# Kernel optimization log

Hardware: AMD Instinct MI355X
Metric: run time of the kernel (lower is better)

Reference implementation:

```python
import jax, jax.numpy as jnp
import numpy as np

N, E, F_IN, EDIM, HEADS, DIM = 100000, 1600000, 128, 16, 4, 16
HC = HEADS * DIM


def add_self_loops_mean(src, dst, ea, n):
    # PyG add_self_loops with fill_value='mean': self-loop edge_attr is the mean
    # of incoming-edge attrs per target node (0 for isolated nodes).
    cnt = jax.ops.segment_sum(jnp.ones((dst.shape[0],), ea.dtype), dst, num_segments=n)
    sm = jax.ops.segment_sum(ea, dst, num_segments=n)
    loop = jnp.where(cnt[:, None] > 0, sm / jnp.maximum(cnt, 1.0)[:, None], 0.0)
    idx = jnp.arange(n, dtype=src.dtype)
    return (jnp.concatenate([src, idx]), jnp.concatenate([dst, idx]),
            jnp.concatenate([ea, loop], axis=0))


def gatv2(x, src, dst, ea, Wl, bl, Wr, br, We, att, bias):
    n = x.shape[0]
    h, c = att.shape
    xl = (x @ Wl + bl).reshape(n, h, c)   # source transform (lin_l)
    xr = (x @ Wr + br).reshape(n, h, c)   # target transform (lin_r)
    ee = (ea @ We).reshape(-1, h, c)      # edge transform (lin_edge, no bias)
    s = jax.nn.leaky_relu(xl[src] + xr[dst] + ee, negative_slope=0.2)  # [E,h,c]
    alpha = jnp.einsum('ehc,hc->eh', s, att)                           # [E,h]
    amax = jax.ops.segment_max(alpha, dst, num_segments=n)
    amax = jnp.where(jnp.isfinite(amax), amax, 0.0)
    ex = jnp.exp(alpha - amax[dst])
    denom = jax.ops.segment_sum(ex, dst, num_segments=n)
    a = ex / (denom[dst] + 1e-16)                                      # segment softmax
    out = jax.ops.segment_sum(xl[src] * a[:, :, None], dst, num_segments=n)
    return out.reshape(n, h * c) + bias


def setup_inputs() -> dict:
    key = jax.random.key(0)
    ks = jax.random.split(key, 24)
    s = 0.1
    d = {
        'x': jax.random.normal(ks[0], (N, F_IN), jnp.float32),
        'edge_index': jax.random.randint(ks[1], (2, E), 0, N, jnp.int32),
        'edge_attr': jax.random.normal(ks[2], (E, EDIM), jnp.float32),
        'Wl1': jax.random.normal(ks[3], (F_IN, HC)) * s, 'bl1': jnp.zeros((HC,)),
        'Wr1': jax.random.normal(ks[4], (F_IN, HC)) * s, 'br1': jnp.zeros((HC,)),
        'We1': jax.random.normal(ks[5], (EDIM, HC)) * s,
        'att1': jax.random.normal(ks[6], (HEADS, DIM)) * s,
        'bias1': jnp.zeros((HC,)),
        'Wl2': jax.random.normal(ks[7], (HC, HC)) * s, 'bl2': jnp.zeros((HC,)),
        'Wr2': jax.random.normal(ks[8], (HC, HC)) * s, 'br2': jnp.zeros((HC,)),
        'We2': jax.random.normal(ks[9], (EDIM, HC)) * s,
        'att2': jax.random.normal(ks[10], (HEADS, DIM)) * s,
        'bias2': jnp.zeros((HC,)),
        'W_lin1': jax.random.normal(ks[11], (HC, DIM)) * s, 'b_lin1': jnp.zeros((DIM,)),
        'W_lin2': jax.random.normal(ks[12], (DIM, 1)) * s, 'b_lin2': jnp.zeros((1,)),
    }
    return d


def reference(x, edge_index, edge_attr, Wl1, bl1, Wr1, br1, We1, att1, bias1,
              Wl2, bl2, Wr2, br2, We2, att2, bias2,
              W_lin1, b_lin1, W_lin2, b_lin2):
    src, dst, ea = add_self_loops_mean(edge_index[0], edge_index[1], edge_attr, x.shape[0])
    h = jax.nn.relu(gatv2(x, src, dst, ea, Wl1, bl1, Wr1, br1, We1, att1, bias1))
    h = jax.nn.relu(gatv2(h, src, dst, ea, Wl2, bl2, Wr2, br2, We2, att2, bias2))
    h = jax.nn.relu(h @ W_lin1 + b_lin1)
    # dropout p=0.1 is identity in eval mode
    out = jax.nn.sigmoid((h @ W_lin2 + b_lin2)[:, 0])
    return out
```

## Files before the change

### kernel.cpp

```cpp
#include <hip/hip_runtime.h>
#include <stdint.h>

typedef unsigned short u16;
typedef unsigned int u32;
typedef unsigned long long u64;

typedef __attribute__((ext_vector_type(8))) short bfrag;
typedef __attribute__((ext_vector_type(4))) float f32x4;

__device__ __forceinline__ float bf2f(u16 u) { return __uint_as_float(((u32)u) << 16); }
__device__ __forceinline__ u16 f2bf(float f) {
    u32 i = __float_as_uint(f);
    u32 r = i + 0x7fffu + ((i >> 16) & 1u);
    return (u16)(r >> 16);
}
__device__ __forceinline__ u32 pack2(float a, float b) {
    return (u32)f2bf(a) | ((u32)f2bf(b) << 16);
}
__device__ __forceinline__ float lo16(u32 u) { return __uint_as_float(u << 16); }
__device__ __forceinline__ float hi16(u32 u) { return __uint_as_float(u & 0xffff0000u); }
#define RFL(x) __builtin_amdgcn_readfirstlane(x)

#define DPP_ROR_ADD(p, ctrl) \
    p += __int_as_float(__builtin_amdgcn_update_dpp(0, __float_as_int(p), ctrl, 0xF, 0xF, false))
__device__ __forceinline__ float red16(float p) {
    DPP_ROR_ADD(p, 0x128);
    DPP_ROR_ADD(p, 0x124);
    DPP_ROR_ADD(p, 0x122);
    DPP_ROR_ADD(p, 0x121);
    return p;
}

__global__ void rank_hist(const int* __restrict__ dst, int E,
                          int* __restrict__ deg, int* __restrict__ rank) {
    int e = blockIdx.x * blockDim.x + threadIdx.x;
    if (e < E) rank[e] = atomicAdd(&deg[dst[e]], 1);
}

#define SCAN_T 256
#define SCAN_E 8
#define SCAN_CHUNK 2048

__global__ void scan_partial(const int* __restrict__ deg, int n, int* __restrict__ partials) {
    __shared__ int sh[SCAN_T];
    int b = blockIdx.x, t = threadIdx.x;
    int base = b * SCAN_CHUNK + t * SCAN_E;
    int s = 0;
#pragma unroll
    for (int i = 0; i < SCAN_E; i++) { int idx = base + i; if (idx < n) s += deg[idx]; }
    sh[t] = s; __syncthreads();
    for (int off = SCAN_T / 2; off > 0; off >>= 1) {
        if (t < off) sh[t] += sh[t + off];
        __syncthreads();
    }
    if (t == 0) partials[b] = sh[0];
}

__global__ void scan_mid(int* __restrict__ partials, int nb) {
    if (threadIdx.x == 0 && blockIdx.x == 0) {
        int acc = 0;
        for (int i = 0; i < nb; i++) { int v = partials[i]; partials[i] = acc; acc += v; }
    }
}

__global__ void scan_final(const int* __restrict__ deg, int n, const int* __restrict__ partials,
                           int* __restrict__ offs, int E) {
    __shared__ int sh[SCAN_T];
    int b = blockIdx.x, t = threadIdx.x;
    int base = b * SCAN_CHUNK + t * SCAN_E;
    int loc[SCAN_E];
    int s = 0;
#pragma unroll
    for (int i = 0; i < SCAN_E; i++) {
        int idx = base + i;
        int v = (idx < n) ? deg[idx] : 0;
        loc[i] = s; s += v;
    }
    sh[t] = s; __syncthreads();
    for (int off = 1; off < SCAN_T; off <<= 1) {
        int v = 0;
        if (t >= off) v = sh[t - off];
        __syncthreads();
        if (t >= off) sh[t] += v;
        __syncthreads();
    }
    int tbase = partials[b] + sh[t] - s;
#pragma unroll
    for (int i = 0; i < SCAN_E; i++) { int idx = base + i; if (idx < n) offs[idx] = tbase + loc[i]; }
    if (b == gridDim.x - 1 && t == SCAN_T - 1) offs[n] = E;
}

__global__ void csr_fill_idx(const int* __restrict__ srcv, const int* __restrict__ dstv,
                             const int* __restrict__ rank,
                             const int* __restrict__ offs, int E,
                             int2* __restrict__ cse) {
    int e = blockIdx.x * blockDim.x + threadIdx.x;
    if (e >= E) return;
    int d = dstv[e];
    int p = offs[d] + rank[e];
    cse[p] = make_int2(srcv[e], e);
}

__global__ void conv_attr(const float4* __restrict__ ea, int E, uint4* __restrict__ eattr) {
    int e = blockIdx.x * blockDim.x + threadIdx.x;
    if (e >= E) return;
    const float4* s = ea + (u64)e * 4;
    float4 v0 = s[0], v1 = s[1], v2 = s[2], v3 = s[3];
    eattr[(u64)e * 2]     = make_uint4(pack2(v0.x, v0.y), pack2(v0.z, v0.w),
                                       pack2(v1.x, v1.y), pack2(v1.z, v1.w));
    eattr[(u64)e * 2 + 1] = make_uint4(pack2(v2.x, v2.y), pack2(v2.z, v2.w),
                                       pack2(v3.x, v3.y), pack2(v3.z, v3.w));
}

template <int K>
__global__ void pack_w(const float* __restrict__ Wl, const float* __restrict__ Wr,
                       u32* __restrict__ Wb) {
    constexpr int NKS = K / 32;
    int t = blockIdx.x * blockDim.x + threadIdx.x;
    if (t >= 8 * NKS * 64) return;
    int lane = t & 63;
    int ks = (t >> 6) % NKS;
    int ct = (t >> 6) / NKS;
    int n = lane & 15, quad = lane >> 4;
    int c = ct * 16 + n;
    const float* W = (c < 64) ? Wl : Wr;
    int cc = c & 63;
    u32* d = Wb + (u64)t * 4;
#pragma unroll
    for (int p = 0; p < 4; p++) {
        int k0 = ks * 32 + quad * 8 + 2 * p;
        d[p] = pack2(W[(u64)k0 * 64 + cc], W[(u64)(k0 + 1) * 64 + cc]);
    }
}

__global__ void pack_we(const float* __restrict__ We, u32* __restrict__ web) {
    int t = blockIdx.x * blockDim.x + threadIdx.x;
    if (t >= 256) return;
    int lane = t & 63, ct = t >> 6;
    int n = lane & 15, quad = lane >> 4;
    int c = ct * 16 + n;
    u32* d = web + (u64)t * 4;
#pragma unroll
    for (int p = 0; p < 4; p++) {
        int k0 = quad * 8 + 2 * p;
        d[p] = (k0 + 1 < 16) ? pack2(We[(u64)k0 * 64 + c], We[(u64)(k0 + 1) * 64 + c]) : 0u;
    }
}

template <int K, bool XF32>
__global__ __launch_bounds__(256) void gemm_mfma(const void* __restrict__ Xv,
                                                 const u32* __restrict__ Wb,
                                                 const float* __restrict__ bl,
                                                 const float* __restrict__ br,
                                                 int N, u16* __restrict__ xl, u16* __restrict__ xr) {
    constexpr int NKS = K / 32;
    int lane = threadIdx.x & 63;
    int gw = (blockIdx.x * 256 + threadIdx.x) >> 6;
    int row0 = gw * 16;
    if (row0 >= N) return;
    int m = lane & 15, quad = lane >> 4;

    f32x4 acc[8];
#pragma unroll
    for (int ct = 0; ct < 8; ct++) acc[ct] = (f32x4){0.f, 0.f, 0.f, 0.f};

#pragma unroll
    for (int ks = 0; ks < NKS; ks++) {
        bfrag a;
        if (XF32) {
            const float* xp = (const float*)Xv + (u64)(row0 + m) * K + ks * 32 + quad * 8;
            float4 v0 = *(const float4*)xp;
            float4 v1 = *(const float4*)(xp + 4);
            union { bfrag v; u32 d[4]; } au;
            au.d[0] = pack2(v0.x, v0.y); au.d[1] = pack2(v0.z, v0.w);
            au.d[2] = pack2(v1.x, v1.y); au.d[3] = pack2(v1.z, v1.w);
            a = au.v;
        } else {
            a = *(const bfrag*)((const u16*)Xv + (u64)(row0 + m) * K + ks * 32 + quad * 8);
        }
#pragma unroll
        for (int ct = 0; ct < 8; ct++) {
            bfrag b = *(const bfrag*)(Wb + (u64)((ct * NKS + ks) * 64 + lane) * 4);
            acc[ct] = __builtin_amdgcn_mfma_f32_16x16x32_bf16(a, b, acc[ct], 0, 0, 0);
        }
    }

    float bvl[4], bvr[4];
#pragma unroll
    for (int ct = 0; ct < 4; ct++) { bvl[ct] = bl[ct * 16 + m]; bvr[ct] = br[ct * 16 + m]; }
#pragma unroll
    for (int r = 0; r < 4; r++) {
        int row = row0 + quad * 4 + r;
        uint2 ql, qr;
        ql.x = pack2(acc[0][r] + bvl[0], acc[1][r] + bvl[1]);
        ql.y = pack2(acc[2][r] + bvl[2], acc[3][r] + bvl[3]);
        qr.x = pack2(acc[4][r] + bvr[0], acc[5][r] + bvr[1]);
        qr.y = pack2(acc[6][r] + bvr[2], acc[7][r] + bvr[3]);
        *(uint2*)(xl + (u64)row * 64 + m * 4) = ql;
        *(uint2*)(xr + (u64)row * 64 + m * 4) = qr;
    }
}

__global__ __launch_bounds__(256) void gat_layer(const u16* __restrict__ xl, const u16* __restrict__ xr,
                                                 const int* __restrict__ offs,
                                                 const int2* __restrict__ cse,
                                                 const u32* __restrict__ eattr,
                                                 const u32* __restrict__ web,
                                                 const float* __restrict__ att,
                                                 const float* __restrict__ bias,
                                                 int N, u16* __restrict__ out) {
    const float LOG2E = 1.44269504088896340736f;
    int l = threadIdx.x & 63;
    int m = l & 15, quad = l >> 4;
    int wid = RFL((int)((blockIdx.x * 256 + threadIdx.x) >> 6));
    int nw = gridDim.x * 4;

    bfrag wb[4];
#pragma unroll
    for (int ct = 0; ct < 4; ct++) wb[ct] = *(const bfrag*)(web + (u64)(ct * 64 + l) * 4);

    float att_l = att[l] * LOG2E;
    float att_f[4];
#pragma unroll
    for (int ct = 0; ct < 4; ct++) att_f[ct] = att[ct * 16 + m] * LOG2E;
    float bias_l = bias[l];

    for (int n = wid; n < N; n += nw) {
        int a = RFL(offs[n]);
        int b = RFL(offs[n + 1]);
        float xr_l = bf2f(xr[(u32)(n * 64 + m * 4 + quad)]);
        float xl_self = bf2f(xl[(u32)(n * 64 + m * 4 + quad)]);
        uint2 qxr = *(const uint2*)(xr + (u32)(n * 64 + m * 4));
        float xr_f[4] = {lo16(qxr.x), hi16(qxr.x), lo16(qxr.y), hi16(qxr.y)};

        float o_f[4] = {0.f, 0.f, 0.f, 0.f};
        float ls_f[4] = {0.f, 0.f, 0.f, 0.f};
        float ee_f[4] = {0.f, 0.f, 0.f, 0.f};

        for (int base = a; base < b; base += 64) {
            int cnt64 = b - base; if (cnt64 > 64) cnt64 = 64;
            int idx = base + l;
            int2 sev = cse[idx < b ? idx : b - 1];
            int sv = sev.x, ev = sev.y;

            for (int j = 0; j < cnt64; j += 16) {
                int cnt = cnt64 - j; if (cnt > 16) cnt = 16;
                int em = __shfl(ev, j + m);
                union { bfrag v; u32 d[4]; } au;
                au.d[0] = 0; au.d[1] = 0; au.d[2] = 0; au.d[3] = 0;
                if (quad < 2 && m < cnt)
                    au.v = *(const bfrag*)(eattr + (u64)em * 8 + quad * 4);
                int jq = j + quad * 4;
                int sr0 = __shfl(sv, jq);
                int sr1 = __shfl(sv, jq + 1);
                int sr2 = __shfl(sv, jq + 2);
                int sr3 = __shfl(sv, jq + 3);
                uint2 g0 = *(const uint2*)(xl + (u32)(sr0 * 64 + m * 4));
                uint2 g1 = *(const uint2*)(xl + (u32)(sr1 * 64 + m * 4));
                uint2 g2 = *(const uint2*)(xl + (u32)(sr2 * 64 + m * 4));
                uint2 g3 = *(const uint2*)(xl + (u32)(sr3 * 64 + m * 4));
                float xv[4][4];
                xv[0][0] = lo16(g0.x); xv[0][1] = hi16(g0.x); xv[0][2] = lo16(g0.y); xv[0][3] = hi16(g0.y);
                xv[1][0] = lo16(g1.x); xv[1][1] = hi16(g1.x); xv[1][2] = lo16(g1.y); xv[1][3] = hi16(g1.y);
                xv[2][0] = lo16(g2.x); xv[2][1] = hi16(g2.x); xv[2][2] = lo16(g2.y); xv[2][3] = hi16(g2.y);
                xv[3][0] = lo16(g3.x); xv[3][1] = hi16(g3.x); xv[3][2] = lo16(g3.y); xv[3][3] = hi16(g3.y);
                f32x4 ee[4];
#pragma unroll
                for (int ct = 0; ct < 4; ct++) {
                    f32x4 c = (f32x4){xr_f[ct], xr_f[ct], xr_f[ct], xr_f[ct]};
                    ee[ct] = __builtin_amdgcn_mfma_f32_16x16x32_bf16(au.v, wb[ct], c, 0, 0, 0);
                }
#pragma unroll
                for (int ct = 0; ct < 4; ct++)
                    ee_f[ct] += (ee[ct][0] + ee[ct][1]) + (ee[ct][2] + ee[ct][3]) - 4.f * xr_f[ct];
                float zz[4][4];
#pragma unroll
                for (int ct = 0; ct < 4; ct++) {
#pragma unroll
                    for (int r = 0; r < 4; r++) {
                        float z = ee[ct][r] + xv[r][ct];
                        z = fmaxf(z, 0.2f * z);
                        zz[ct][r] = z * att_f[ct];
                    }
                }
#define R16(ctrl) { \
    DPP_ROR_ADD(zz[0][0], ctrl); DPP_ROR_ADD(zz[0][1], ctrl); DPP_ROR_ADD(zz[0][2], ctrl); DPP_ROR_ADD(zz[0][3], ctrl); \
    DPP_ROR_ADD(zz[1][0], ctrl); DPP_ROR_ADD(zz[1][1], ctrl); DPP_ROR_ADD(zz[1][2], ctrl); DPP_ROR_ADD(zz[1][3], ctrl); \
    DPP_ROR_ADD(zz[2][0], ctrl); DPP_ROR_ADD(zz[2][1], ctrl); DPP_ROR_ADD(zz[2][2], ctrl); DPP_ROR_ADD(zz[2][3], ctrl); \
    DPP_ROR_ADD(zz[3][0], ctrl); DPP_ROR_ADD(zz[3][1], ctrl); DPP_ROR_ADD(zz[3][2], ctrl); DPP_ROR_ADD(zz[3][3], ctrl); }
                R16(0x128) R16(0x124) R16(0x122) R16(0x121)
#undef R16
                float w[4][4];
#pragma unroll
                for (int ct = 0; ct < 4; ct++) {
#pragma unroll
                    for (int r = 0; r < 4; r++)
                        asm("v_exp_f32 %0, %1" : "=v"(w[ct][r]) : "v"(zz[ct][r]));
                }
                if (cnt < 16) {
#pragma unroll
                    for (int r = 0; r < 4; r++) {
                        bool ok = (quad * 4 + r) < cnt;
#pragma unroll
                        for (int ct = 0; ct < 4; ct++) w[ct][r] = ok ? w[ct][r] : 0.f;
                    }
                }
#pragma unroll
                for (int ct = 0; ct < 4; ct++) {
#pragma unroll
                    for (int r = 0; r < 4; r++) {
                        ls_f[ct] += w[ct][r];
                        o_f[ct] = fmaf(w[ct][r], xv[r][ct], o_f[ct]);
                    }
                }
            }
        }

#pragma unroll
        for (int ct = 0; ct < 4; ct++) {
            o_f[ct] += __shfl_xor(o_f[ct], 16);  o_f[ct] += __shfl_xor(o_f[ct], 32);
            ls_f[ct] += __shfl_xor(ls_f[ct], 16); ls_f[ct] += __shfl_xor(ls_f[ct], 32);
            ee_f[ct] += __shfl_xor(ee_f[ct], 16); ee_f[ct] += __shfl_xor(ee_f[ct], 32);
        }
        float o    = (quad & 2) ? ((quad & 1) ? o_f[3] : o_f[2]) : ((quad & 1) ? o_f[1] : o_f[0]);
        float lsum = (quad & 2) ? ((quad & 1) ? ls_f[3] : ls_f[2]) : ((quad & 1) ? ls_f[1] : ls_f[0]);
        float eesum= (quad & 2) ? ((quad & 1) ? ee_f[3] : ee_f[2]) : ((quad & 1) ? ee_f[1] : ee_f[0]);

        int deg = b - a;
        float inv = (deg > 0) ? 1.f / (float)deg : 0.f;
        float z = (eesum * inv + xr_l) + xl_self;
        z = fmaxf(z, 0.2f * z);
        float vv = red16(z * att_l);
        float ws;
        asm("v_exp_f32 %0, %1" : "=v"(ws) : "v"(vv));
        lsum += ws;
        o = fmaf(ws, xl_self, o);

        float res = o / (lsum + 1e-16f) + bias_l;
        res = fmaxf(res, 0.f);
        out[(u32)(n * 64 + l)] = f2bf(res);
    }
}

__global__ __launch_bounds__(256) void mlp_head(const u16* __restrict__ h,
                                                const float* __restrict__ W1, const float* __restrict__ b1,
                                                const float* __restrict__ W2, const float* __restrict__ b2,
                                                int N, float* __restrict__ out) {
    __shared__ float w1[64 * 16];
    __shared__ float sb1[16];
    __shared__ float w2[16];
    for (int i = threadIdx.x; i < 64 * 16; i += 256) w1[i] = W1[i];
    if (threadIdx.x < 16) { sb1[threadIdx.x] = b1[threadIdx.x]; w2[threadIdx.x] = W2[threadIdx.x]; }
    __syncthreads();
    float b2v = b2[0];
    int n = blockIdx.x * blockDim.x + threadIdx.x;
    if (n < N) {
        float hv[64];
        const u32* hp = (const u32*)(h + (u64)n * 64);
#pragma unroll
        for (int i = 0; i < 32; i++) { u32 u = hp[i]; hv[2 * i] = lo16(u); hv[2 * i + 1] = hi16(u); }
        float z = b2v;
        for (int j = 0; j < 16; j++) {
            float acc = sb1[j];
#pragma unroll
            for (int k = 0; k < 64; k++) acc = fmaf(hv[k], w1[k * 16 + j], acc);
            acc = fmaxf(acc, 0.f);
            z = fmaf(acc, w2[j], z);
        }
        out[n] = 1.f / (1.f + __expf(-z));
    }
}

extern "C" void kernel_launch(void* const* d_in, const int* in_sizes, int n_in,
                              void* d_out, int out_size, void* d_ws, size_t ws_size,
                              hipStream_t stream) {
    const float* x    = (const float*)d_in[0];
    const int*   ei   = (const int*)d_in[1];
    const float* ea   = (const float*)d_in[2];
    const float* Wl1  = (const float*)d_in[3];
    const float* bl1  = (const float*)d_in[4];
    const float* Wr1  = (const float*)d_in[5];
    const float* br1  = (const float*)d_in[6];
    const float* We1  = (const float*)d_in[7];
    const float* att1 = (const float*)d_in[8];
    const float* bias1= (const float*)d_in[9];
    const float* Wl2  = (const float*)d_in[10];
    const float* bl2  = (const float*)d_in[11];
    const float* Wr2  = (const float*)d_in[12];
    const float* br2  = (const float*)d_in[13];
    const float* We2  = (const float*)d_in[14];
    const float* att2 = (const float*)d_in[15];
    const float* bias2= (const float*)d_in[16];
    const float* W1   = (const float*)d_in[17];
    const float* b1   = (const float*)d_in[18];
    const float* W2   = (const float*)d_in[19];
    const float* b2   = (const float*)d_in[20];
    float* out = (float*)d_out;

    const int N = in_sizes[0] / 128;
    const int E = in_sizes[1] / 2;
    const int* srcv = ei;
    const int* dstv = ei + E;

    uint8_t* p = (uint8_t*)d_ws;
    auto carve = [&](size_t bytes) -> void* {
        void* r = (void*)p;
        p += (bytes + 255) & ~(size_t)255;
        return r;
    };
    int*  deg     = (int*)carve((size_t)N * 4);
    int*  rank    = (int*)carve((size_t)E * 4);
    int*  offs    = (int*)carve((size_t)(N + 1) * 4);
    int*  partials= (int*)carve(4096);
    int2* cse     = (int2*)carve((size_t)E * 8);
    u32*  eattr   = (u32*)carve((size_t)E * 32);
    u16*  xl      = (u16*)carve((size_t)N * 64 * 2);
    u16*  xr      = (u16*)carve((size_t)N * 64 * 2);
    u16*  hb      = (u16*)carve((size_t)N * 64 * 2);
    u32*  wb1     = (u32*)carve(8 * 4 * 64 * 16);
    u32*  wb2     = (u32*)carve(8 * 2 * 64 * 16);
    u32*  web1    = (u32*)carve(4 * 64 * 4 * 4);
    u32*  web2    = (u32*)carve(4 * 64 * 4 * 4);
    (void)ws_size; (void)n_in; (void)out_size;

    hipMemsetAsync(deg, 0, (size_t)N * 4, stream);

    const int B = 256;
    pack_w<128><<<8, 256, 0, stream>>>(Wl1, Wr1, wb1);
    pack_w<64><<<4, 256, 0, stream>>>(Wl2, Wr2, wb2);
    pack_we<<<1, 256, 0, stream>>>(We1, web1);
    pack_we<<<1, 256, 0, stream>>>(We2, web2);
    conv_attr<<<(E + B - 1) / B, B, 0, stream>>>((const float4*)ea, E, (uint4*)eattr);

    rank_hist<<<(E + B - 1) / B, B, 0, stream>>>(dstv, E, deg, rank);
    int nb = (N + SCAN_CHUNK - 1) / SCAN_CHUNK;
    scan_partial<<<nb, SCAN_T, 0, stream>>>(deg, N, partials);
    scan_mid<<<1, 64, 0, stream>>>(partials, nb);
    scan_final<<<nb, SCAN_T, 0, stream>>>(deg, N, partials, offs, E);
    csr_fill_idx<<<(E + B - 1) / B, B, 0, stream>>>(srcv, dstv, rank, offs, E, cse);

    int gemm_blocks = (N / 16 + 3) / 4;
    gemm_mfma<128, true><<<gemm_blocks, 256, 0, stream>>>(x, wb1, bl1, br1, N, xl, xr);
    gat_layer<<<8192, 256, 0, stream>>>(xl, xr, offs, cse, eattr, web1,
                                        att1, bias1, N, hb);
    gemm_mfma<64, false><<<gemm_blocks, 256, 0, stream>>>(hb, wb2, bl2, br2, N, xl, xr);
    gat_layer<<<8192, 256, 0, stream>>>(xl, xr, offs, cse, eattr, web2,
                                        att2, bias2, N, hb);
    mlp_head<<<(N + B - 1) / B, B, 0, stream>>>(hb, W1, b1, W2, b2, N, out);
}
```

Baseline: 602.4 us.

## Store edge attributes in CSR order and merge weight-packing kernels

Edge attributes are now converted to bf16 and written in destination-sorted CSR order. Source indices are stored the same way, so the GAT layers read attributes contiguously instead of gathering them by edge id through a shuffle. The CSR build now does a scatter of edge ids followed by a gather pass that reads the fp32 attributes randomly. The four small weight-packing launches are merged into one kernel. The cost is an extra kernel and random reads during preprocessing, traded for sequential loads in both attention layers.

```diff
diff --git a/kernel.cpp b/kernel.cpp
--- a/kernel.cpp
+++ b/kernel.cpp
@@ -90,34 +90,33 @@
     if (b == gridDim.x - 1 && t == SCAN_T - 1) offs[n] = E;
 }
 
-__global__ void csr_fill_idx(const int* __restrict__ srcv, const int* __restrict__ dstv,
-                             const int* __restrict__ rank,
-                             const int* __restrict__ offs, int E,
-                             int2* __restrict__ cse) {
+__global__ void fill_eid(const int* __restrict__ dstv,
+                         const int* __restrict__ rank,
+                         const int* __restrict__ offs, int E,
+                         int* __restrict__ ceid) {
     int e = blockIdx.x * blockDim.x + threadIdx.x;
     if (e >= E) return;
-    int d = dstv[e];
-    int p = offs[d] + rank[e];
-    cse[p] = make_int2(srcv[e], e);
-}
-
-__global__ void conv_attr(const float4* __restrict__ ea, int E, uint4* __restrict__ eattr) {
-    int e = blockIdx.x * blockDim.x + threadIdx.x;
-    if (e >= E) return;
+    ceid[offs[dstv[e]] + rank[e]] = e;
+}
+
+__global__ void gather_fill(const int* __restrict__ ceid,
+                            const int* __restrict__ srcv,
+                            const float4* __restrict__ ea, int E,
+                            int* __restrict__ csrc, uint4* __restrict__ cattr) {
+    int p = blockIdx.x * blockDim.x + threadIdx.x;
+    if (p >= E) return;
+    int e = ceid[p];
     const float4* s = ea + (u64)e * 4;
     float4 v0 = s[0], v1 = s[1], v2 = s[2], v3 = s[3];
-    eattr[(u64)e * 2]     = make_uint4(pack2(v0.x, v0.y), pack2(v0.z, v0.w),
+    cattr[(u64)p * 2]     = make_uint4(pack2(v0.x, v0.y), pack2(v0.z, v0.w),
                                        pack2(v1.x, v1.y), pack2(v1.z, v1.w));
-    eattr[(u64)e * 2 + 1] = make_uint4(pack2(v2.x, v2.y), pack2(v2.z, v2.w),
+    cattr[(u64)p * 2 + 1] = make_uint4(pack2(v2.x, v2.y), pack2(v2.z, v2.w),
                                        pack2(v3.x, v3.y), pack2(v3.z, v3.w));
-}
-
-template <int K>
-__global__ void pack_w(const float* __restrict__ Wl, const float* __restrict__ Wr,
-                       u32* __restrict__ Wb) {
-    constexpr int NKS = K / 32;
-    int t = blockIdx.x * blockDim.x + threadIdx.x;
-    if (t >= 8 * NKS * 64) return;
+    csrc[p] = srcv[e];
+}
+
+__device__ __forceinline__ void pack_w_job(const float* Wl, const float* Wr, u32* Wb,
+                                           int t, int NKS) {
     int lane = t & 63;
     int ks = (t >> 6) % NKS;
     int ct = (t >> 6) / NKS;
@@ -132,10 +131,7 @@
         d[p] = pack2(W[(u64)k0 * 64 + cc], W[(u64)(k0 + 1) * 64 + cc]);
     }
 }
-
-__global__ void pack_we(const float* __restrict__ We, u32* __restrict__ web) {
-    int t = blockIdx.x * blockDim.x + threadIdx.x;
-    if (t >= 256) return;
+__device__ __forceinline__ void pack_we_job(const float* We, u32* web, int t) {
     int lane = t & 63, ct = t >> 6;
     int n = lane & 15, quad = lane >> 4;
     int c = ct * 16 + n;
@@ -145,6 +141,17 @@
         int k0 = quad * 8 + 2 * p;
         d[p] = (k0 + 1 < 16) ? pack2(We[(u64)k0 * 64 + c], We[(u64)(k0 + 1) * 64 + c]) : 0u;
     }
+}
+__global__ void pack_all(const float* __restrict__ Wl1, const float* __restrict__ Wr1,
+                         const float* __restrict__ Wl2, const float* __restrict__ Wr2,
+                         const float* __restrict__ We1, const float* __restrict__ We2,
+                         u32* __restrict__ wb1, u32* __restrict__ wb2,
+                         u32* __restrict__ web1, u32* __restrict__ web2) {
+    int t = blockIdx.x * blockDim.x + threadIdx.x;
+    if (t < 2048)       pack_w_job(Wl1, Wr1, wb1, t, 4);
+    else if (t < 3072)  pack_w_job(Wl2, Wr2, wb2, t - 2048, 2);
+    else if (t < 3328)  pack_we_job(We1, web1, t - 3072);
+    else if (t < 3584)  pack_we_job(We2, web2, t - 3328);
 }
 
 template <int K, bool XF32>
@@ -203,8 +210,8 @@
 
 __global__ __launch_bounds__(256) void gat_layer(const u16* __restrict__ xl, const u16* __restrict__ xr,
                                                  const int* __restrict__ offs,
-                                                 const int2* __restrict__ cse,
-                                                 const u32* __restrict__ eattr,
+                                                 const int* __restrict__ csrc,
+                                                 const u32* __restrict__ cattr,
                                                  const u32* __restrict__ web,
                                                  const float* __restrict__ att,
                                                  const float* __restrict__ bias,
@@ -240,16 +247,14 @@
         for (int base = a; base < b; base += 64) {
             int cnt64 = b - base; if (cnt64 > 64) cnt64 = 64;
             int idx = base + l;
-            int2 sev = cse[idx < b ? idx : b - 1];
-            int sv = sev.x, ev = sev.y;
+            int sv = csrc[idx < b ? idx : b - 1];
 
             for (int j = 0; j < cnt64; j += 16) {
                 int cnt = cnt64 - j; if (cnt > 16) cnt = 16;
-                int em = __shfl(ev, j + m);
                 union { bfrag v; u32 d[4]; } au;
                 au.d[0] = 0; au.d[1] = 0; au.d[2] = 0; au.d[3] = 0;
                 if (quad < 2 && m < cnt)
-                    au.v = *(const bfrag*)(eattr + (u64)em * 8 + quad * 4);
+                    au.v = *(const bfrag*)(cattr + (u64)(base + j + m) * 8 + quad * 4);
                 int jq = j + quad * 4;
                 int sr0 = __shfl(sv, jq);
                 int sr1 = __shfl(sv, jq + 1);
@@ -412,8 +417,9 @@
     int*  rank    = (int*)carve((size_t)E * 4);
     int*  offs    = (int*)carve((size_t)(N + 1) * 4);
     int*  partials= (int*)carve(4096);
-    int2* cse     = (int2*)carve((size_t)E * 8);
-    u32*  eattr   = (u32*)carve((size_t)E * 32);
+    int*  ceid    = (int*)carve((size_t)E * 4);
+    int*  csrc    = (int*)carve((size_t)E * 4);
+    u32*  cattr   = (u32*)carve((size_t)E * 32);
     u16*  xl      = (u16*)carve((size_t)N * 64 * 2);
     u16*  xr      = (u16*)carve((size_t)N * 64 * 2);
     u16*  hb      = (u16*)carve((size_t)N * 64 * 2);
@@ -426,25 +432,22 @@
     hipMemsetAsync(deg, 0, (size_t)N * 4, stream);
 
     const int B = 256;
-    pack_w<128><<<8, 256, 0, stream>>>(Wl1, Wr1, wb1);
-    pack_w<64><<<4, 256, 0, stream>>>(Wl2, Wr2, wb2);
-    pack_we<<<1, 256, 0, stream>>>(We1, web1);
-    pack_we<<<1, 256, 0, stream>>>(We2, web2);
-    conv_attr<<<(E + B - 1) / B, B, 0, stream>>>((const float4*)ea, E, (uint4*)eattr);
-
+    pack_all<<<14, 256, 0, stream>>>(Wl1, Wr1, Wl2, Wr2, We1, We2, wb1, wb2, web1, web2);
     rank_hist<<<(E + B - 1) / B, B, 0, stream>>>(dstv, E, deg, rank);
     int nb = (N + SCAN_CHUNK - 1) / SCAN_CHUNK;
     scan_partial<<<nb, SCAN_T, 0, stream>>>(deg, N, partials);
     scan_mid<<<1, 64, 0, stream>>>(partials, nb);
     scan_final<<<nb, SCAN_T, 0, stream>>>(deg, N, partials, offs, E);
-    csr_fill_idx<<<(E + B - 1) / B, B, 0, stream>>>(srcv, dstv, rank, offs, E, cse);
+    fill_eid<<<(E + B - 1) / B, B, 0, stream>>>(dstv, rank, offs, E, ceid);
+    gather_fill<<<(E + B - 1) / B, B, 0, stream>>>(ceid, srcv, (const float4*)ea, E,
+                                                   csrc, (uint4*)cattr);
 
     int gemm_blocks = (N / 16 + 3) / 4;
     gemm_mfma<128, true><<<gemm_blocks, 256, 0, stream>>>(x, wb1, bl1, br1, N, xl, xr);
-    gat_layer<<<8192, 256, 0, stream>>>(xl, xr, offs, cse, eattr, web1,
+    gat_layer<<<8192, 256, 0, stream>>>(xl, xr, offs, csrc, cattr, web1,
                                         att1, bias1, N, hb);
     gemm_mfma<64, false><<<gemm_blocks, 256, 0, stream>>>(hb, wb2, bl2, br2, N, xl, xr);
-    gat_layer<<<8192, 256, 0, stream>>>(xl, xr, offs, cse, eattr, web2,
+    gat_layer<<<8192, 256, 0, stream>>>(xl, xr, offs, csrc, cattr, web2,
                                         att2, bias2, N, hb);
     mlp_head<<<(N + B - 1) / B, B, 0, stream>>>(hb, W1, b1, W2, b2, N, out);
 }
```

New measurement: 610.7 us. Within noise of the previous version (+1.4%).

## Fuse weight packing kernels and merge edge prep with first GEMM launch

Applied to the files above, without the earlier changes.

Combines the four weight-packing launches into one kernel, and merges the edge-attribute conversion, the degree histogram/rank atomics and the layer-1 GEMM into a single heterogeneous launch, with block roles interleaved 1:4. This is meant to cut launch overhead and let the memory-bound edge work overlap with the MFMA GEMM. The cost is a more complex block-role dispatch, and the uniform launch bounds may hurt occupancy for the edge blocks.

```diff
diff --git a/kernel.cpp b/kernel.cpp
--- a/kernel.cpp
+++ b/kernel.cpp
@@ -31,12 +31,6 @@
     return p;
 }
 
-__global__ void rank_hist(const int* __restrict__ dst, int E,
-                          int* __restrict__ deg, int* __restrict__ rank) {
-    int e = blockIdx.x * blockDim.x + threadIdx.x;
-    if (e < E) rank[e] = atomicAdd(&deg[dst[e]], 1);
-}
-
 #define SCAN_T 256
 #define SCAN_E 8
 #define SCAN_CHUNK 2048
@@ -90,34 +84,17 @@
     if (b == gridDim.x - 1 && t == SCAN_T - 1) offs[n] = E;
 }
 
-__global__ void csr_fill_idx(const int* __restrict__ srcv, const int* __restrict__ dstv,
+__global__ void csr_fill_cse(const int* __restrict__ srcv, const int* __restrict__ dstv,
                              const int* __restrict__ rank,
                              const int* __restrict__ offs, int E,
                              int2* __restrict__ cse) {
     int e = blockIdx.x * blockDim.x + threadIdx.x;
     if (e >= E) return;
-    int d = dstv[e];
-    int p = offs[d] + rank[e];
-    cse[p] = make_int2(srcv[e], e);
-}
-
-__global__ void conv_attr(const float4* __restrict__ ea, int E, uint4* __restrict__ eattr) {
-    int e = blockIdx.x * blockDim.x + threadIdx.x;
-    if (e >= E) return;
-    const float4* s = ea + (u64)e * 4;
-    float4 v0 = s[0], v1 = s[1], v2 = s[2], v3 = s[3];
-    eattr[(u64)e * 2]     = make_uint4(pack2(v0.x, v0.y), pack2(v0.z, v0.w),
-                                       pack2(v1.x, v1.y), pack2(v1.z, v1.w));
-    eattr[(u64)e * 2 + 1] = make_uint4(pack2(v2.x, v2.y), pack2(v2.z, v2.w),
-                                       pack2(v3.x, v3.y), pack2(v3.z, v3.w));
-}
-
-template <int K>
-__global__ void pack_w(const float* __restrict__ Wl, const float* __restrict__ Wr,
-                       u32* __restrict__ Wb) {
-    constexpr int NKS = K / 32;
-    int t = blockIdx.x * blockDim.x + threadIdx.x;
-    if (t >= 8 * NKS * 64) return;
+    cse[offs[dstv[e]] + rank[e]] = make_int2(srcv[e], e);
+}
+
+__device__ __forceinline__ void pack_w_job(const float* Wl, const float* Wr, u32* Wb,
+                                           int t, int NKS) {
     int lane = t & 63;
     int ks = (t >> 6) % NKS;
     int ct = (t >> 6) / NKS;
@@ -132,10 +109,7 @@
         d[p] = pack2(W[(u64)k0 * 64 + cc], W[(u64)(k0 + 1) * 64 + cc]);
     }
 }
-
-__global__ void pack_we(const float* __restrict__ We, u32* __restrict__ web) {
-    int t = blockIdx.x * blockDim.x + threadIdx.x;
-    if (t >= 256) return;
+__device__ __forceinline__ void pack_we_job(const float* We, u32* web, int t) {
     int lane = t & 63, ct = t >> 6;
     int n = lane & 15, quad = lane >> 4;
     int c = ct * 16 + n;
@@ -146,16 +120,27 @@
         d[p] = (k0 + 1 < 16) ? pack2(We[(u64)k0 * 64 + c], We[(u64)(k0 + 1) * 64 + c]) : 0u;
     }
 }
+__global__ void pack_all(const float* __restrict__ Wl1, const float* __restrict__ Wr1,
+                         const float* __restrict__ Wl2, const float* __restrict__ Wr2,
+                         const float* __restrict__ We1, const float* __restrict__ We2,
+                         u32* __restrict__ wb1, u32* __restrict__ wb2,
+                         u32* __restrict__ web1, u32* __restrict__ web2) {
+    int t = blockIdx.x * blockDim.x + threadIdx.x;
+    if (t < 2048)       pack_w_job(Wl1, Wr1, wb1, t, 4);
+    else if (t < 3072)  pack_w_job(Wl2, Wr2, wb2, t - 2048, 2);
+    else if (t < 3328)  pack_we_job(We1, web1, t - 3072);
+    else if (t < 3584)  pack_we_job(We2, web2, t - 3328);
+}
 
 template <int K, bool XF32>
-__global__ __launch_bounds__(256) void gemm_mfma(const void* __restrict__ Xv,
-                                                 const u32* __restrict__ Wb,
-                                                 const float* __restrict__ bl,
-                                                 const float* __restrict__ br,
-                                                 int N, u16* __restrict__ xl, u16* __restrict__ xr) {
+__device__ __forceinline__ void gemm_body(int gblk, const void* __restrict__ Xv,
+                                          const u32* __restrict__ Wb,
+                                          const float* __restrict__ bl,
+                                          const float* __restrict__ br,
+                                          int N, u16* __restrict__ xl, u16* __restrict__ xr) {
     constexpr int NKS = K / 32;
     int lane = threadIdx.x & 63;
-    int gw = (blockIdx.x * 256 + threadIdx.x) >> 6;
+    int gw = gblk * 4 + (threadIdx.x >> 6);
     int row0 = gw * 16;
     if (row0 >= N) return;
     int m = lane & 15, quad = lane >> 4;
@@ -198,6 +183,42 @@
         qr.y = pack2(acc[6][r] + bvr[2], acc[7][r] + bvr[3]);
         *(uint2*)(xl + (u64)row * 64 + m * 4) = ql;
         *(uint2*)(xr + (u64)row * 64 + m * 4) = qr;
+    }
+}
+
+__global__ __launch_bounds__(256) void gemm_mfma64(const u16* __restrict__ Xv,
+                                                   const u32* __restrict__ Wb,
+                                                   const float* __restrict__ bl,
+                                                   const float* __restrict__ br,
+                                                   int N, u16* __restrict__ xl, u16* __restrict__ xr) {
+    gemm_body<64, false>(blockIdx.x, Xv, Wb, bl, br, N, xl, xr);
+}
+
+__global__ __launch_bounds__(256) void prep_gemm1(const int* __restrict__ dstv,
+                                                  const float4* __restrict__ ea, int E,
+                                                  int* __restrict__ deg, int* __restrict__ rank,
+                                                  uint4* __restrict__ eattr,
+                                                  const float* __restrict__ x,
+                                                  const u32* __restrict__ wb1,
+                                                  const float* __restrict__ bl1,
+                                                  const float* __restrict__ br1,
+                                                  int N, u16* __restrict__ xl, u16* __restrict__ xr) {
+    int g = blockIdx.x / 5;
+    int r = blockIdx.x % 5;
+    if (r == 0) {
+        gemm_body<128, true>(g, x, wb1, bl1, br1, N, xl, xr);
+    } else {
+        int e = (g * 4 + (r - 1)) * 256 + threadIdx.x;
+        if (e >= E) return;
+        const float4* s = ea + (u64)e * 4;
+        float4 v0 = s[0], v1 = s[1], v2 = s[2], v3 = s[3];
+        int d = dstv[e];
+        int rk = atomicAdd(&deg[d], 1);
+        eattr[(u64)e * 2]     = make_uint4(pack2(v0.x, v0.y), pack2(v0.z, v0.w),
+                                           pack2(v1.x, v1.y), pack2(v1.z, v1.w));
+        eattr[(u64)e * 2 + 1] = make_uint4(pack2(v2.x, v2.y), pack2(v2.z, v2.w),
+                                           pack2(v3.x, v3.y), pack2(v3.z, v3.w));
+        rank[e] = rk;
     }
 }
 
@@ -426,24 +447,23 @@
     hipMemsetAsync(deg, 0, (size_t)N * 4, stream);
 
     const int B = 256;
-    pack_w<128><<<8, 256, 0, stream>>>(Wl1, Wr1, wb1);
-    pack_w<64><<<4, 256, 0, stream>>>(Wl2, Wr2, wb2);
-    pack_we<<<1, 256, 0, stream>>>(We1, web1);
-    pack_we<<<1, 256, 0, stream>>>(We2, web2);
-    conv_attr<<<(E + B - 1) / B, B, 0, stream>>>((const float4*)ea, E, (uint4*)eattr);
-
-    rank_hist<<<(E + B - 1) / B, B, 0, stream>>>(dstv, E, deg, rank);
+    pack_all<<<14, 256, 0, stream>>>(Wl1, Wr1, Wl2, Wr2, We1, We2, wb1, wb2, web1, web2);
+
+    int gemm_blocks = (N / 16 + 3) / 4;
+    int edge_blocks = (E + B - 1) / B;
+    int gmax = gemm_blocks > (edge_blocks + 3) / 4 ? gemm_blocks : (edge_blocks + 3) / 4;
+    prep_gemm1<<<gmax * 5, 256, 0, stream>>>(dstv, (const float4*)ea, E, deg, rank,
+                                             (uint4*)eattr, x, wb1, bl1, br1, N, xl, xr);
+
     int nb = (N + SCAN_CHUNK - 1) / SCAN_CHUNK;
     scan_partial<<<nb, SCAN_T, 0, stream>>>(deg, N, partials);
     scan_mid<<<1, 64, 0, stream>>>(partials, nb);
     scan_final<<<nb, SCAN_T, 0, stream>>>(deg, N, partials, offs, E);
-    csr_fill_idx<<<(E + B - 1) / B, B, 0, stream>>>(srcv, dstv, rank, offs, E, cse);
-
-    int gemm_blocks = (N / 16 + 3) / 4;
-    gemm_mfma<128, true><<<gemm_blocks, 256, 0, stream>>>(x, wb1, bl1, br1, N, xl, xr);
+    csr_fill_cse<<<edge_blocks, B, 0, stream>>>(srcv, dstv, rank, offs, E, cse);
+
     gat_layer<<<8192, 256, 0, stream>>>(xl, xr, offs, cse, eattr, web1,
                                         att1, bias1, N, hb);
-    gemm_mfma<64, false><<<gemm_blocks, 256, 0, stream>>>(hb, wb2, bl2, br2, N, xl, xr);
+    gemm_mfma64<<<gemm_blocks, 256, 0, stream>>>(hb, wb2, bl2, br2, N, xl, xr);
     gat_layer<<<8192, 256, 0, stream>>>(xl, xr, offs, cse, eattr, web2,
                                         att2, bias2, N, hb);
     mlp_head<<<(N + B - 1) / B, B, 0, stream>>>(hb, W1, b1, W2, b2, N, out);
```

After: 541.5 us. -10.1%, faster.
